# Optimization experiments

Hardware: AMD Instinct MI355X
Metric: run time of the kernel (lower is better)

Reference implementation:

```python
import jax, jax.numpy as jnp
import numpy as np

B, N, D = 16, 16384, 256
H, W = 128, 128  # N == H*W: coords cover the grid exactly once (collision-free scatter)
K = 3


def setup_inputs() -> dict:
    key = jax.random.key(0)
    k1, k2, k3, k4 = jax.random.split(key, 4)
    x = jax.random.normal(k1, (B, N, D), dtype=jnp.float32)
    # coords: per-batch random permutation of all grid cells -> unique (gx, gy) per batch
    perm = jax.vmap(lambda k: jax.random.permutation(k, H * W))(jax.random.split(k2, B))  # (B, N)
    gx = perm % W
    gy = perm // W
    coords = jnp.stack([gx, gy], axis=-1).astype(jnp.int32)  # (B, N, 2), [...,0]=x, [...,1]=y
    # depthwise Conv2d params: weight (D, 1, K, K), bias (D,)  (torch kaiming-uniform-ish scale)
    bound = 1.0 / np.sqrt(K * K)
    conv_w = jax.random.uniform(k3, (D, 1, K, K), minval=-bound, maxval=bound, dtype=jnp.float32)
    conv_b = jax.random.uniform(k4, (D,), minval=-bound, maxval=bound, dtype=jnp.float32)
    return {"x": x, "coords": coords, "conv_w": conv_w, "conv_b": conv_b}


def reference(x, coords, conv_w, conv_b):
    b, n, d = x.shape
    # normalize coords to zero-based bounding box (per batch min, as in torch)
    min_c = coords.min(axis=1, keepdims=True)
    gc = coords - min_c
    max_c = gc.max(axis=1).max(axis=0)
    Hh = int(max_c[1]) + 1
    Ww = int(max_c[0]) + 1
    if Hh * Ww > 256 * 256:
        return x  # safety guard: skip mixing
    gx = gc[..., 0]
    gy = gc[..., 1]
    flat = gy * Ww + gx  # (B, N) flattened spatial index
    x_T = jnp.swapaxes(x, 1, 2)  # (B, D, N)
    # scatter: (B, D, H*W) dense grid, one vmap'd scatter per batch element
    scatter = lambda xt, f: jnp.zeros((d, Hh * Ww), x.dtype).at[:, f].set(xt)
    grid = jax.vmap(scatter)(x_T, flat).reshape(b, d, Hh, Ww)
    # depthwise conv (groups = D) with SAME-style padding k//2, then exact (erf) GELU
    out_grid = jax.lax.conv_general_dilated(
        grid, conv_w,
        window_strides=(1, 1),
        padding=[(K // 2, K // 2), (K // 2, K // 2)],
        feature_group_count=d,
    ) + conv_b[None, :, None, None]
    out_grid = jax.nn.gelu(out_grid, approximate=False)
    # gather back at the same positions, residual add
    out_flat = out_grid.reshape(b, d, Hh * Ww)
    gathered = jax.vmap(lambda g, f: g[:, f])(out_flat, flat)  # (B, D, N)
    return x + jnp.swapaxes(gathered, 1, 2)
```

## Files before the change

kernel.cpp:

```cpp
#include <hip/hip_runtime.h>
#include <hip/hip_bf16.h>

#define BB 16
#define NN 16384
#define GW 128
#define TSX 16
#define TSY 8
#define HSX 18
#define HSY 10

typedef float f32x4 __attribute__((ext_vector_type(4)));

__global__ __launch_bounds__(256) void build_inv_kernel(
    const int* __restrict__ coords, int* __restrict__ inv,
    float* __restrict__ zrow) {
  int i = blockIdx.x * blockDim.x + threadIdx.x;
  int b = i >> 14;
  int gx = coords[2 * (size_t)i];
  int gy = coords[2 * (size_t)i + 1];
  inv[(b << 14) + (gy << 7) + gx] = i & (NN - 1);
  if (blockIdx.x == 0) zrow[threadIdx.x] = 0.0f;
}

__device__ __forceinline__ float gelu_fast(float a) {
  const float s = a * a;
  const float t = fmaf(0.044715f * a, s, a);
  const float e = __builtin_amdgcn_exp2f(t * -2.3022083f);
  return a * __builtin_amdgcn_rcpf(1.0f + e);
}

#define LCOL(j, col)                                                      \
  _Pragma("unroll") for (int r4 = 0; r4 < 4; ++r4) {                      \
    const int n_ = __builtin_amdgcn_readfirstlane(s_inv[r0 + r4][j]);     \
    const float* p_ = (n_ >= 0) ? xb + ((size_t)n_ << 8) : zrow;          \
    col[r4] = *(const f32x4*)(p_ + c4);                                   \
  }

__global__ __launch_bounds__(256) void mixer_kernel(
    const float* __restrict__ x, const float* __restrict__ cw,
    const float* __restrict__ cb, const int* __restrict__ inv,
    const float* __restrict__ zrow, float* __restrict__ out) {
  __shared__ int s_inv[HSY][HSX];

  const int id = blockIdx.x;
  const int rem = id >> 3;
  const int b = ((id & 7) << 1) + (rem >> 7);
  const int tile = rem & 127;
  const int gy0 = (tile >> 3) * TSY;
  const int gx0 = (tile & 7) * TSX;

  const int tid = threadIdx.x;
  const int lane = tid & 63;
  const int wv = tid >> 6;
  const int c4 = lane << 2;

  if (tid < HSY * HSX) {
    const int wy = tid / HSX, wx = tid - wy * HSX;
    const int gy = gy0 - 1 + wy, gx = gx0 - 1 + wx;
    int nv = -1;
    if ((unsigned)gy < (unsigned)GW && (unsigned)gx < (unsigned)GW)
      nv = inv[(b << 14) + (gy << 7) + gx];
    s_inv[wy][wx] = nv;
  }

  f32x4 wq[9], bq;
#pragma unroll
  for (int cc = 0; cc < 4; ++cc) {
    bq[cc] = cb[c4 + cc];
#pragma unroll
    for (int j = 0; j < 9; ++j) wq[j][cc] = cw[(c4 + cc) * 9 + j];
  }
  __syncthreads();

  const float* __restrict__ xb = x + ((size_t)b << 22);
  float* __restrict__ ob = out + ((size_t)b << 22);
  const int r0 = wv << 1;

  f32x4 cA[4], cB[4], cC[4], cD[4];
  LCOL(0, cA)
  LCOL(1, cB)
  LCOL(2, cC)
#pragma unroll
  for (int j = 2; j < HSX; ++j) {
    if (j + 1 < HSX) { LCOL(j + 1, cD) }
    __builtin_amdgcn_sched_barrier(0);

#pragma unroll
    for (int rr = 0; rr < 2; ++rr) {
      f32x4 a = bq;
      a += wq[0] * cA[rr];
      a += wq[1] * cB[rr];
      a += wq[2] * cC[rr];
      a += wq[3] * cA[rr + 1];
      a += wq[4] * cB[rr + 1];
      a += wq[5] * cC[rr + 1];
      a += wq[6] * cA[rr + 2];
      a += wq[7] * cB[rr + 2];
      a += wq[8] * cC[rr + 2];
      f32x4 res;
#pragma unroll
      for (int cc = 0; cc < 4; ++cc)
        res[cc] = cB[rr + 1][cc] + gelu_fast(a[cc]);
      const int n = __builtin_amdgcn_readfirstlane(s_inv[r0 + rr + 1][j - 1]);
      __builtin_nontemporal_store(res, (f32x4*)(ob + ((size_t)n << 8) + c4));
    }
#pragma unroll
    for (int r4 = 0; r4 < 4; ++r4) {
      cA[r4] = cB[r4];
      cB[r4] = cC[r4];
      cC[r4] = cD[r4];
    }
  }
}

extern "C" void kernel_launch(void* const* d_in, const int* in_sizes, int n_in,
                              void* d_out, int out_size, void* d_ws,
                              size_t ws_size, hipStream_t stream) {
  const float* x = (const float*)d_in[0];
  const int* coords = (const int*)d_in[1];
  const float* cw = (const float*)d_in[2];
  const float* cb = (const float*)d_in[3];
  float* out = (float*)d_out;
  int* inv = (int*)d_ws;
  float* zrow = (float*)d_ws + (size_t)BB * NN;

  {
    dim3 grid((BB * NN) / 256), block(256);
    build_inv_kernel<<<grid, block, 0, stream>>>(coords, inv, zrow);
  }
  {
    dim3 grid(BB * (GW / TSY) * (GW / TSX)), block(256);
    mixer_kernel<<<grid, block, 0, stream>>>(x, cw, cb, inv, zrow, out);
  }
}
```

Before: 108.9 us.

## Shrink tile to one row per wave, hold indices in registers, prefetch two columns

Tile height drops from 8 to 4 rows, so each wave now computes one output row instead of two, and the grid doubles in size. The shared-memory index table and its __syncthreads are replaced by a per-wave register of halo indices read with readlane. The column pipeline now prefetches two columns ahead instead of one. The aim is to remove block-level sync and LDS traffic and to deepen load overlap. In exchange, each wave reloads 3 halo rows for every 1 output row instead of 4 for 2, which raises redundant global reads of x.

```diff
diff --git a/kernel.cpp b/kernel.cpp
--- a/kernel.cpp
+++ b/kernel.cpp
@@ -5,9 +5,9 @@
 #define NN 16384
 #define GW 128
 #define TSX 16
-#define TSY 8
+#define TSY 4
 #define HSX 18
-#define HSY 10
+#define HSY 6
 
 typedef float f32x4 __attribute__((ext_vector_type(4)));
 
@@ -29,23 +29,23 @@
   return a * __builtin_amdgcn_rcpf(1.0f + e);
 }
 
+#define HIDX(k) __builtin_amdgcn_readlane(vIdx, (k))
+
 #define LCOL(j, col)                                                      \
-  _Pragma("unroll") for (int r4 = 0; r4 < 4; ++r4) {                      \
-    const int n_ = __builtin_amdgcn_readfirstlane(s_inv[r0 + r4][j]);     \
+  _Pragma("unroll") for (int r3 = 0; r3 < 3; ++r3) {                      \
+    const int n_ = HIDX(r3 * HSX + (j));                                  \
     const float* p_ = (n_ >= 0) ? xb + ((size_t)n_ << 8) : zrow;          \
-    col[r4] = *(const f32x4*)(p_ + c4);                                   \
+    col[r3] = *(const f32x4*)(p_ + c4);                                   \
   }
 
 __global__ __launch_bounds__(256) void mixer_kernel(
     const float* __restrict__ x, const float* __restrict__ cw,
     const float* __restrict__ cb, const int* __restrict__ inv,
     const float* __restrict__ zrow, float* __restrict__ out) {
-  __shared__ int s_inv[HSY][HSX];
-
   const int id = blockIdx.x;
   const int rem = id >> 3;
-  const int b = ((id & 7) << 1) + (rem >> 7);
-  const int tile = rem & 127;
+  const int b = ((id & 7) << 1) + (rem >> 8);
+  const int tile = rem & 255;
   const int gy0 = (tile >> 3) * TSY;
   const int gx0 = (tile & 7) * TSX;
 
@@ -53,14 +53,16 @@
   const int lane = tid & 63;
   const int wv = tid >> 6;
   const int c4 = lane << 2;
+  const int r0 = wv;
 
-  if (tid < HSY * HSX) {
-    const int wy = tid / HSX, wx = tid - wy * HSX;
-    const int gy = gy0 - 1 + wy, gx = gx0 - 1 + wx;
-    int nv = -1;
-    if ((unsigned)gy < (unsigned)GW && (unsigned)gx < (unsigned)GW)
-      nv = inv[(b << 14) + (gy << 7) + gx];
-    s_inv[wy][wx] = nv;
+  const int* __restrict__ invb = inv + (b << 14);
+  int vIdx;
+  {
+    const int r_ = lane / HSX, j_ = lane - r_ * HSX;
+    const int gy_ = gy0 - 1 + r0 + r_, gx_ = gx0 - 1 + j_;
+    vIdx = (lane < 3 * HSX && (unsigned)gy_ < (unsigned)GW &&
+            (unsigned)gx_ < (unsigned)GW)
+               ? invb[(gy_ << 7) + gx_] : -1;
   }
 
   f32x4 wq[9], bq;
@@ -70,45 +72,44 @@
 #pragma unroll
     for (int j = 0; j < 9; ++j) wq[j][cc] = cw[(c4 + cc) * 9 + j];
   }
-  __syncthreads();
 
   const float* __restrict__ xb = x + ((size_t)b << 22);
   float* __restrict__ ob = out + ((size_t)b << 22);
-  const int r0 = wv << 1;
 
-  f32x4 cA[4], cB[4], cC[4], cD[4];
+  f32x4 cA[3], cB[3], cC[3], cD[3], cE[3];
   LCOL(0, cA)
   LCOL(1, cB)
   LCOL(2, cC)
+  LCOL(3, cD)
 #pragma unroll
   for (int j = 2; j < HSX; ++j) {
-    if (j + 1 < HSX) { LCOL(j + 1, cD) }
+    if (j + 2 < HSX) { LCOL(j + 2, cE) }
     __builtin_amdgcn_sched_barrier(0);
 
-#pragma unroll
-    for (int rr = 0; rr < 2; ++rr) {
+    {
       f32x4 a = bq;
-      a += wq[0] * cA[rr];
-      a += wq[1] * cB[rr];
-      a += wq[2] * cC[rr];
-      a += wq[3] * cA[rr + 1];
-      a += wq[4] * cB[rr + 1];
-      a += wq[5] * cC[rr + 1];
-      a += wq[6] * cA[rr + 2];
-      a += wq[7] * cB[rr + 2];
-      a += wq[8] * cC[rr + 2];
+      a += wq[0] * cA[0];
+      a += wq[1] * cB[0];
+      a += wq[2] * cC[0];
+      a += wq[3] * cA[1];
+      a += wq[4] * cB[1];
+      a += wq[5] * cC[1];
+      a += wq[6] * cA[2];
+      a += wq[7] * cB[2];
+      a += wq[8] * cC[2];
       f32x4 res;
 #pragma unroll
       for (int cc = 0; cc < 4; ++cc)
-        res[cc] = cB[rr + 1][cc] + gelu_fast(a[cc]);
-      const int n = __builtin_amdgcn_readfirstlane(s_inv[r0 + rr + 1][j - 1]);
+        res[cc] = cB[1][cc] + gelu_fast(a[cc]);
+      const int n = HIDX(HSX + (j - 1));
       __builtin_nontemporal_store(res, (f32x4*)(ob + ((size_t)n << 8) + c4));
     }
 #pragma unroll
-    for (int r4 = 0; r4 < 4; ++r4) {
-      cA[r4] = cB[r4];
-      cB[r4] = cC[r4];
-      cC[r4] = cD[r4];
+    for (int r3 = 0; r3 < 3; ++r3) {
+      cA[r3] = cB[r3];
+      cB[r3] = cC[r3];
+      cC[r3] = cD[r3];
+      cD[r3] = cE[r3];
     }
   }
 }
```

Result: slower. 119.4 us (+9.6%).
